# Kernel tuning notes

Measured on AMD Instinct MI355X. Metric: run time of the kernel, lower is better.

The kernel has to match this reference:

```python
import jax, jax.numpy as jnp
import numpy as np

B, Hh, Ww, C = 2, 224, 224, 768
NB, BS, M = 8, 96, 96  # n_blocks, block_size, truncated modes (M == BS required by source reshape)


def setup_inputs() -> dict:
    key = jax.random.key(0)
    k0, k1, k2 = jax.random.split(key, 3)
    x = jax.random.normal(k0, (B, Hh * Ww, C), jnp.float32)
    block_weights = jax.random.normal(k1, (NB, BS, BS), jnp.float32) * 0.02
    block_bias = jnp.zeros((NB, BS), jnp.float32)
    gates = jnp.full((NB,), 0.5, jnp.float32)
    proj_w = jax.random.normal(k2, (C, C), jnp.float32) * 0.02  # nn.Linear weight (out, in)
    proj_b = jnp.zeros((C,), jnp.float32)
    rescale = jnp.float32(0.1)
    return {"x": x, "block_weights": block_weights, "block_bias": block_bias,
            "gates": gates, "proj_w": proj_w, "proj_b": proj_b, "rescale": rescale}


def reference(x, block_weights, block_bias, gates, proj_w, proj_b, rescale):
    b, n, c = x.shape
    # (B, N, C) -> (B, C, H, W) -> (B, NB, BS, H, W); no channel padding (NB*BS == C)
    xi = x.reshape(b, Hh, Ww, c).transpose(0, 3, 1, 2).reshape(b, NB, BS, Hh, Ww)
    # ortho-normalized 2D rFFT over (H, W): (B, NB, BS, H, W//2+1) complex
    xf = jnp.fft.rfft2(xi, norm='ortho')
    trunc = xf[..., :M]  # keep first M frequency modes along last axis
    # Per-block linear mixing along the MODE axis (faithful to source reshape),
    # bias added to both real and imaginary parts, as in the original.
    out_r = jnp.einsum('abchm,bmk->abchk', trunc.real, block_weights) + block_bias[None, :, None, None, :]
    out_i = jnp.einsum('abchm,bmk->abchk', trunc.imag, block_weights) + block_bias[None, :, None, None, :]
    g = jax.nn.sigmoid(gates)[None, :, None, None, None]  # shrinkage gate per block
    out = (out_r * g) + 1j * (out_i * g)
    xf_new = xf.at[..., :M].set(out)
    xs = jnp.fft.irfft2(xf_new, s=(Hh, Ww), norm='ortho')  # (B, NB, BS, H, W)
    # merge blocks -> (B, N, C)
    x_out = xs.reshape(b, NB * BS, Hh, Ww).transpose(0, 2, 3, 1).reshape(b, Hh * Ww, c)
    x_proj = (x_out @ proj_w.T + proj_b) * rescale
    return x_proj + x_out
```

## Files before the change

kernel.cpp:

```cpp
#include <hip/hip_runtime.h>
#include <hip/hip_bf16.h>

#define HH 224
#define WWN 224
#define CCH 768
#define NBLK 8
#define BSZ 96
#define PI2_N 0.0280499344f

typedef short v8s __attribute__((ext_vector_type(8)));
typedef float v4f __attribute__((ext_vector_type(4)));

__device__ inline float bf2f(short s) {
    unsigned int u = ((unsigned int)(unsigned short)s) << 16;
    return __builtin_bit_cast(float, u);
}
__device__ inline short f2bf(float f) {
    unsigned int u = __builtin_bit_cast(unsigned int, f);
    u = (u + 0x7FFFu + ((u >> 16) & 1u)) >> 16;
    return (short)u;
}

__global__ __launch_bounds__(224) void k_build_U(const float* __restrict__ bw,
                                                 float* __restrict__ A1,
                                                 float* __restrict__ A2) {
    __shared__ float cosT[224], sinT[224], Wcol[96];
    int blk = blockIdx.x / 96, k = blockIdx.x % 96;
    int t = threadIdx.x;
    float ang = (float)t * PI2_N;
    cosT[t] = cosf(ang); sinT[t] = sinf(ang);
    if (t < 96) Wcol[t] = bw[(blk * 96 + t) * 96 + k];
    __syncthreads();
    float s1 = 0.f, s2 = 0.f;
    int u = t;
    for (int m = 0; m < 96; ++m) {
        int idx = (m * u) % 224;
        s1 += Wcol[m] * cosT[idx];
        s2 += Wcol[m] * sinT[idx];
    }
    A1[(blk * 96 + k) * 224 + u] = s1;
    A2[(blk * 96 + k) * 224 + u] = s2;
}

__global__ __launch_bounds__(224) void k_build_T(const float* __restrict__ A1,
                                                 const float* __restrict__ A2,
                                                 const float* __restrict__ gates,
                                                 const float* __restrict__ bias,
                                                 short* __restrict__ T,
                                                 float* __restrict__ V) {
    __shared__ float cosT[224], sinT[224], ck[96], sk[96];
    int blk = blockIdx.x / 224, w = blockIdx.x % 224;
    int t = threadIdx.x;
    float ang = (float)t * PI2_N;
    cosT[t] = cosf(ang); sinT[t] = sinf(ang);
    __syncthreads();
    if (t < 96) {
        float a = (t == 0) ? 1.f : 2.f;
        int idx = (t * w) % 224;
        ck[t] = a * cosT[idx];
        sk[t] = a * sinT[idx];
    }
    __syncthreads();
    float g = 1.f / (1.f + expf(-gates[blk]));
    int u = t;
    float s = 0.f;
    for (int k = 0; k < 96; ++k)
        s += ck[k] * A1[(blk * 96 + k) * 224 + u] + sk[k] * A2[(blk * 96 + k) * 224 + u];
    int dw = (w - u + 224) % 224;
    float p = 0.f;
    for (int k = 96; k < 113; ++k) {
        float a = (k == 112) ? 1.f : 2.f;
        p += a * cosT[(k * dw) % 224];
    }
    T[blk * 50176 + w * 224 + u] = f2bf((g * s + p) * (1.f / 224.f));
    if (t == 0) {
        float vs = 0.f;
        for (int k = 0; k < 96; ++k) vs += bias[blk * 96 + k] * (ck[k] - sk[k]);
        V[blk * 224 + w] = g * vs;
    }
}

__global__ void k_cvt_pw(const float* __restrict__ pw, short* __restrict__ pwb, int n) {
    int i = blockIdx.x * 256 + threadIdx.x;
    if (i < n) pwb[i] = f2bf(pw[i]);
}

__global__ __launch_bounds__(256, 2) void k_spectral(const float* __restrict__ x,
                                                     const short* __restrict__ T,
                                                     const float* __restrict__ V,
                                                     short* __restrict__ XB) {
    __shared__ short XT[96 * 232];
    int id = blockIdx.x;
    int blk = id & 7;
    int h = (id >> 3) % 224;
    int b = id / (8 * 224);
    const float* xp = x + (size_t)(b * 224 + h) * 224 * 768 + blk * 96;
    int tid = threadIdx.x;
    for (int idx = tid; idx < 224 * 24; idx += 256) {
        int u = idx / 24, c4 = (idx % 24) * 4;
        float4 vv = *(const float4*)(xp + u * 768 + c4);
        XT[(c4 + 0) * 232 + u] = f2bf(vv.x);
        XT[(c4 + 1) * 232 + u] = f2bf(vv.y);
        XT[(c4 + 2) * 232 + u] = f2bf(vv.z);
        XT[(c4 + 3) * 232 + u] = f2bf(vv.w);
    }
    __syncthreads();
    int lane = tid & 63, wave = tid >> 6;
    int q = lane >> 4, ln = lane & 15;
    v4f acc[4][6];
    #pragma unroll
    for (int i = 0; i < 4; ++i)
        #pragma unroll
        for (int ct = 0; ct < 6; ++ct) acc[i][ct] = {0.f, 0.f, 0.f, 0.f};
    const short* Tb = T + blk * 50176;
    #pragma unroll
    for (int ks = 0; ks < 7; ++ks) {
        int k0 = ks * 32 + q * 8;
        v8s a[4];
        #pragma unroll
        for (int i = 0; i < 4; ++i) {
            int wt = wave + 4 * i;
            int row = (wt < 14 ? wt : 13) * 16 + ln;
            a[i] = *(const v8s*)(Tb + row * 224 + k0);
        }
        #pragma unroll
        for (int ct = 0; ct < 6; ++ct) {
            v8s bfr = *(const v8s*)(&XT[(ct * 16 + ln) * 232 + k0]);
            #pragma unroll
            for (int i = 0; i < 4; ++i)
                acc[i][ct] = __builtin_amdgcn_mfma_f32_16x16x32_bf16(a[i], bfr, acc[i][ct], 0, 0, 0);
        }
    }
    short* XBp = XB + (size_t)(b * 224 + h) * 224 * 768 + blk * 96;
    #pragma unroll
    for (int i = 0; i < 4; ++i) {
        int wt = wave + 4 * i;
        if (wt < 14) {
            #pragma unroll
            for (int reg = 0; reg < 4; ++reg) {
                int ww = wt * 16 + q * 4 + reg;
                float vadd = (h == 0) ? V[blk * 224 + ww] : 0.f;
                #pragma unroll
                for (int ct = 0; ct < 6; ++ct)
                    XBp[(size_t)ww * 768 + ct * 16 + ln] = f2bf(acc[i][ct][reg] + vadd);
            }
        }
    }
}

__global__ __launch_bounds__(256, 2) void k_gemm(const short* __restrict__ XB,
                                                 const short* __restrict__ PWB,
                                                 const float* __restrict__ pb,
                                                 const float* __restrict__ rescale,
                                                 float* __restrict__ out) {
    __shared__ short As[128 * 72], Bs[128 * 72];
    int id = blockIdx.x;
    int mblk = id / 6, nblk = id % 6;
    int m0 = mblk * 128, n0 = nblk * 128;
    int tid = threadIdx.x;
    int lane = tid & 63, wave = tid >> 6;
    int q = lane >> 4, ln = lane & 15;
    int wm = (wave & 1) * 64, wn = (wave >> 1) * 64;
    v4f acc[4][4];
    #pragma unroll
    for (int mt = 0; mt < 4; ++mt)
        #pragma unroll
        for (int nt = 0; nt < 4; ++nt) acc[mt][nt] = {0.f, 0.f, 0.f, 0.f};
    for (int kb = 0; kb < 12; ++kb) {
        int k0 = kb * 64;
        #pragma unroll
        for (int j = 0; j < 4; ++j) {
            int cid = j * 256 + tid;
            int row = cid >> 3, kc = (cid & 7) * 8;
            *(v8s*)(As + row * 72 + kc) = *(const v8s*)(XB + (size_t)(m0 + row) * 768 + k0 + kc);
            *(v8s*)(Bs + row * 72 + kc) = *(const v8s*)(PWB + (size_t)(n0 + row) * 768 + k0 + kc);
        }
        __syncthreads();
        #pragma unroll
        for (int k2 = 0; k2 < 2; ++k2) {
            int kk = k2 * 32 + q * 8;
            v8s a[4], bfr[4];
            #pragma unroll
            for (int mt = 0; mt < 4; ++mt) a[mt] = *(const v8s*)(As + (wm + mt * 16 + ln) * 72 + kk);
            #pragma unroll
            for (int nt = 0; nt < 4; ++nt) bfr[nt] = *(const v8s*)(Bs + (wn + nt * 16 + ln) * 72 + kk);
            #pragma unroll
            for (int mt = 0; mt < 4; ++mt)
                #pragma unroll
                for (int nt = 0; nt < 4; ++nt)
                    acc[mt][nt] = __builtin_amdgcn_mfma_f32_16x16x32_bf16(a[mt], bfr[nt], acc[mt][nt], 0, 0, 0);
        }
        __syncthreads();
    }
    float rs = rescale[0];
    float pbv[4];
    #pragma unroll
    for (int nt = 0; nt < 4; ++nt) pbv[nt] = pb[n0 + wn + nt * 16 + ln];
    #pragma unroll
    for (int mt = 0; mt < 4; ++mt)
        #pragma unroll
        for (int reg = 0; reg < 4; ++reg) {
            int r = m0 + wm + mt * 16 + q * 4 + reg;
            #pragma unroll
            for (int nt = 0; nt < 4; ++nt) {
                int c = n0 + wn + nt * 16 + ln;
                float resid = bf2f(XB[(size_t)r * 768 + c]);
                out[(size_t)r * 768 + c] = resid + rs * (acc[mt][nt][reg] + pbv[nt]);
            }
        }
}

extern "C" void kernel_launch(void* const* d_in, const int* in_sizes, int n_in,
                              void* d_out, int out_size, void* d_ws, size_t ws_size,
                              hipStream_t stream) {
    const float* x      = (const float*)d_in[0];
    const float* bw     = (const float*)d_in[1];
    const float* bias   = (const float*)d_in[2];
    const float* gates  = (const float*)d_in[3];
    const float* pw     = (const float*)d_in[4];
    const float* pb     = (const float*)d_in[5];
    const float* rescale= (const float*)d_in[6];
    float* out = (float*)d_out;
    char* ws = (char*)d_ws;
    short* T   = (short*)(ws + 0);
    short* PWB = (short*)(ws + 802816);
    float* V   = (float*)(ws + 1982464);
    float* A1  = (float*)(ws + 1989632);
    float* A2  = (float*)(ws + 2677760);
    short* XB  = (short*)(ws + 3366912);

    k_build_U<<<dim3(768), dim3(224), 0, stream>>>(bw, A1, A2);
    k_build_T<<<dim3(1792), dim3(224), 0, stream>>>(A1, A2, gates, bias, T, V);
    k_cvt_pw<<<dim3(2304), dim3(256), 0, stream>>>(pw, PWB, 768 * 768);
    k_spectral<<<dim3(2 * 224 * 8), dim3(256), 0, stream>>>(x, T, V, XB);
    k_gemm<<<dim3(784 * 6), dim3(256), 0, stream>>>(XB, PWB, pb, rescale, out);
}
```

Before: 820.0 us.

## Load GEMM tiles via direct global-to-LDS with XOR swizzle, remap blocks per XCD

```diff
diff --git a/kernel.cpp b/kernel.cpp
--- a/kernel.cpp
+++ b/kernel.cpp
@@ -1,11 +1,6 @@
 #include <hip/hip_runtime.h>
 #include <hip/hip_bf16.h>
 
-#define HH 224
-#define WWN 224
-#define CCH 768
-#define NBLK 8
-#define BSZ 96
 #define PI2_N 0.0280499344f
 
 typedef short v8s __attribute__((ext_vector_type(8)));
@@ -19,6 +14,11 @@
     unsigned int u = __builtin_bit_cast(unsigned int, f);
     u = (u + 0x7FFFu + ((u >> 16) & 1u)) >> 16;
     return (short)u;
+}
+__device__ inline void gl_lds16(const short* g, short* l) {
+    __builtin_amdgcn_global_load_lds(
+        (const __attribute__((address_space(1))) void*)g,
+        (__attribute__((address_space(3))) void*)l, 16, 0, 0);
 }
 
 __global__ __launch_bounds__(224) void k_build_U(const float* __restrict__ bw,
@@ -96,13 +96,19 @@
     int b = id / (8 * 224);
     const float* xp = x + (size_t)(b * 224 + h) * 224 * 768 + blk * 96;
     int tid = threadIdx.x;
-    for (int idx = tid; idx < 224 * 24; idx += 256) {
-        int u = idx / 24, c4 = (idx % 24) * 4;
-        float4 vv = *(const float4*)(xp + u * 768 + c4);
-        XT[(c4 + 0) * 232 + u] = f2bf(vv.x);
-        XT[(c4 + 1) * 232 + u] = f2bf(vv.y);
-        XT[(c4 + 2) * 232 + u] = f2bf(vv.z);
-        XT[(c4 + 3) * 232 + u] = f2bf(vv.w);
+    for (int idx = tid; idx < 112 * 24; idx += 256) {
+        int u2 = idx / 24, c4 = (idx % 24) * 4;
+        int u = u2 * 2;
+        float4 v0 = *(const float4*)(xp + u * 768 + c4);
+        float4 v1 = *(const float4*)(xp + (u + 1) * 768 + c4);
+        unsigned p0 = (unsigned short)f2bf(v0.x) | ((unsigned)(unsigned short)f2bf(v1.x) << 16);
+        unsigned p1 = (unsigned short)f2bf(v0.y) | ((unsigned)(unsigned short)f2bf(v1.y) << 16);
+        unsigned p2 = (unsigned short)f2bf(v0.z) | ((unsigned)(unsigned short)f2bf(v1.z) << 16);
+        unsigned p3 = (unsigned short)f2bf(v0.w) | ((unsigned)(unsigned short)f2bf(v1.w) << 16);
+        *(unsigned*)(&XT[(c4 + 0) * 232 + u]) = p0;
+        *(unsigned*)(&XT[(c4 + 1) * 232 + u]) = p1;
+        *(unsigned*)(&XT[(c4 + 2) * 232 + u]) = p2;
+        *(unsigned*)(&XT[(c4 + 3) * 232 + u]) = p3;
     }
     __syncthreads();
     int lane = tid & 63, wave = tid >> 6;
@@ -153,9 +159,11 @@
                                                  const float* __restrict__ pb,
                                                  const float* __restrict__ rescale,
                                                  float* __restrict__ out) {
-    __shared__ short As[128 * 72], Bs[128 * 72];
+    __shared__ short As[128 * 64], Bs[128 * 64];
     int id = blockIdx.x;
-    int mblk = id / 6, nblk = id % 6;
+    int xcd = id & 7, slot = id >> 3;
+    int mblk = xcd * 98 + slot / 6;
+    int nblk = slot % 6;
     int m0 = mblk * 128, n0 = nblk * 128;
     int tid = threadIdx.x;
     int lane = tid & 63, wave = tid >> 6;
@@ -170,10 +178,11 @@
         int k0 = kb * 64;
         #pragma unroll
         for (int j = 0; j < 4; ++j) {
-            int cid = j * 256 + tid;
-            int row = cid >> 3, kc = (cid & 7) * 8;
-            *(v8s*)(As + row * 72 + kc) = *(const v8s*)(XB + (size_t)(m0 + row) * 768 + k0 + kc);
-            *(v8s*)(Bs + row * 72 + kc) = *(const v8s*)(PWB + (size_t)(n0 + row) * 768 + k0 + kc);
+            int r0 = wave * 32 + j * 8;
+            int row = r0 + (lane >> 3);
+            int col8 = (lane & 7) ^ (row & 7);
+            gl_lds16(XB + (size_t)(m0 + row) * 768 + k0 + col8 * 8, As + r0 * 64);
+            gl_lds16(PWB + (size_t)(n0 + row) * 768 + k0 + col8 * 8, Bs + r0 * 64);
         }
         __syncthreads();
         #pragma unroll
@@ -181,9 +190,15 @@
             int kk = k2 * 32 + q * 8;
             v8s a[4], bfr[4];
             #pragma unroll
-            for (int mt = 0; mt < 4; ++mt) a[mt] = *(const v8s*)(As + (wm + mt * 16 + ln) * 72 + kk);
-            #pragma unroll
-            for (int nt = 0; nt < 4; ++nt) bfr[nt] = *(const v8s*)(Bs + (wn + nt * 16 + ln) * 72 + kk);
+            for (int mt = 0; mt < 4; ++mt) {
+                int r = wm + mt * 16 + ln;
+                a[mt] = *(const v8s*)(As + r * 64 + (kk ^ ((r & 7) * 8)));
+            }
+            #pragma unroll
+            for (int nt = 0; nt < 4; ++nt) {
+                int r = wn + nt * 16 + ln;
+                bfr[nt] = *(const v8s*)(Bs + r * 64 + (kk ^ ((r & 7) * 8)));
+            }
             #pragma unroll
             for (int mt = 0; mt < 4; ++mt)
                 #pragma unroll
```

After: 752.8 us. 8.2% less time.
